# Performance work log

Hardware: AMD Instinct MI355X
Metric: run time of the kernel (lower is better)

The kernel has to match this reference:

```python
import jax, jax.numpy as jnp
import numpy as np
import math

H = 8
D_MODEL = 512
D_K = D_MODEL // H          # 64, per-head value dim
D_QK = D_K // 2             # 32, per-head query/key dim
B, S = 2, 4096


def setup_inputs() -> dict:
    key = jax.random.key(0)
    ks = jax.random.split(key, 20)
    std = 0.02
    inp = {
        'query': jax.random.normal(ks[0], (B, S, D_MODEL), jnp.float32),
        'key':   jax.random.normal(ks[1], (B, S, D_MODEL), jnp.float32),
        'value': jax.random.normal(ks[2], (B, S, D_MODEL), jnp.float32),
        # MLP_q: d_model -> 2*d_model -> d_model/2
        'Wq1': jax.random.normal(ks[3], (D_MODEL, 2 * D_MODEL), jnp.float32) * std,
        'bq1': jnp.zeros((2 * D_MODEL,), jnp.float32),
        'Wq2': jax.random.normal(ks[4], (2 * D_MODEL, D_MODEL // 2), jnp.float32) * std,
        'bq2': jnp.zeros((D_MODEL // 2,), jnp.float32),
        # MLP_k: d_model -> 2*d_model -> d_model/2
        'Wk1': jax.random.normal(ks[5], (D_MODEL, 2 * D_MODEL), jnp.float32) * std,
        'bk1': jnp.zeros((2 * D_MODEL,), jnp.float32),
        'Wk2': jax.random.normal(ks[6], (2 * D_MODEL, D_MODEL // 2), jnp.float32) * std,
        'bk2': jnp.zeros((D_MODEL // 2,), jnp.float32),
        # linear_v and output linear: d_model -> d_model
        'Wv': jax.random.normal(ks[7], (D_MODEL, D_MODEL), jnp.float32) * std,
        'bv': jnp.zeros((D_MODEL,), jnp.float32),
        'Wo': jax.random.normal(ks[8], (D_MODEL, D_MODEL), jnp.float32) * std,
        'bo': jnp.zeros((D_MODEL,), jnp.float32),
    }
    return inp


def reference(query, key, value, Wq1, bq1, Wq2, bq2, Wk1, bk1, Wk2, bk2, Wv, bv, Wo, bo):
    nb = query.shape[0]
    # MLP_q / MLP_k: Linear -> exact GELU -> Linear (torch GELU default is erf)
    q = jax.nn.gelu(query @ Wq1 + bq1, approximate=False) @ Wq2 + bq2   # [B,S,D_MODEL/2]
    k = jax.nn.gelu(key   @ Wk1 + bk1, approximate=False) @ Wk2 + bk2   # [B,S,D_MODEL/2]
    v = value @ Wv + bv                                                  # [B,S,D_MODEL]

    q = q.reshape(nb, -1, H, D_QK)   # [B,S,H,d_qk]
    k = k.reshape(nb, -1, H, D_QK)
    v = v.reshape(nb, -1, H, D_K)    # [B,S,H,d_k]

    # scores scaled by sqrt(d_qk) since query.size(-1) == d_k//2 in the original
    scores = jnp.einsum('bqhd,bkhd->bhqk', q, k) / math.sqrt(D_QK)  # [B,H,S,S]
    p = jax.nn.softmax(scores, axis=-1)
    x = jnp.einsum('bhqk,bkhd->bqhd', p, v).reshape(nb, -1, H * D_K)  # [B,S,D_MODEL]
    return x @ Wo + bo
```

## Files before the change

kernel.cpp:

```cpp
#include <hip/hip_runtime.h>
#include <math.h>

typedef __attribute__((ext_vector_type(8))) short short8;
typedef __bf16 bf16x8 __attribute__((ext_vector_type(8)));
typedef __attribute__((ext_vector_type(4))) float f32x4;
typedef __attribute__((ext_vector_type(16))) float f32x16;
typedef __attribute__((ext_vector_type(4))) unsigned uint4v;

__device__ inline short f2bf(float f) {
    unsigned u = __builtin_bit_cast(unsigned, f);
    u += 0x7fff + ((u >> 16) & 1);
    return (short)(u >> 16);
}
__device__ inline float bf2f(short h) {
    return __builtin_bit_cast(float, ((unsigned)(unsigned short)h) << 16);
}
__device__ inline float gelu_f(float x) {
    return 0.5f * x * (1.f + erff(x * 0.70710678118654752f));
}

__global__ __launch_bounds__(256) void prep_all(
    const float* __restrict__ q, const float* __restrict__ k,
    const float* __restrict__ v,
    short* __restrict__ qc, short* __restrict__ kc, short* __restrict__ vc,
    const float* __restrict__ Wq1, const float* __restrict__ Wk1,
    const float* __restrict__ Wq2, const float* __restrict__ Wk2,
    const float* __restrict__ Wv,  const float* __restrict__ Wo,
    short* __restrict__ Wq1t, short* __restrict__ Wk1t,
    short* __restrict__ Wq2t, short* __restrict__ Wk2t,
    short* __restrict__ Wvt,  short* __restrict__ Wot)
{
    int id = blockIdx.x;
    if (id < 6144) {
        const float* src = id < 2048 ? q : (id < 4096 ? k : v);
        short* dst = id < 2048 ? qc : (id < 4096 ? kc : vc);
        int blk = id & 2047;
        size_t i = ((size_t)blk * 256 + threadIdx.x) * 8;
        float4 a = *(const float4*)(src + i);
        float4 b = *(const float4*)(src + i + 4);
        short8 o;
        o[0] = f2bf(a.x); o[1] = f2bf(a.y); o[2] = f2bf(a.z); o[3] = f2bf(a.w);
        o[4] = f2bf(b.x); o[5] = f2bf(b.y); o[6] = f2bf(b.z); o[7] = f2bf(b.w);
        *(short8*)(void*)(dst + i) = o;
        return;
    }
    id -= 6144;
    const float* W; short* Wt; int K, N;
    if (id < 512)       { W = Wq1; Wt = Wq1t; K = 512;  N = 1024; }
    else if (id < 1024) { W = Wk1; Wt = Wk1t; K = 512;  N = 1024; id -= 512; }
    else if (id < 1280) { W = Wq2; Wt = Wq2t; K = 1024; N = 256;  id -= 1024; }
    else if (id < 1536) { W = Wk2; Wt = Wk2t; K = 1024; N = 256;  id -= 1280; }
    else if (id < 1792) { W = Wv;  Wt = Wvt;  K = 512;  N = 512;  id -= 1536; }
    else                { W = Wo;  Wt = Wot;  K = 512;  N = 512;  id -= 1792; }
    int nx = N >> 5;
    int n0 = (id % nx) * 32, k0 = (id / nx) * 32;

    __shared__ float T[32][33];
    int tid = threadIdx.x;
    int r = tid >> 3, c4 = (tid & 7) * 4;
    float4 v4 = *(const float4*)&W[(size_t)(k0 + r) * N + n0 + c4];
    T[r][c4 + 0] = v4.x; T[r][c4 + 1] = v4.y; T[r][c4 + 2] = v4.z; T[r][c4 + 3] = v4.w;
    __syncthreads();
    short4 o;
    o.x = f2bf(T[c4 + 0][r]);
    o.y = f2bf(T[c4 + 1][r]);
    o.z = f2bf(T[c4 + 2][r]);
    o.w = f2bf(T[c4 + 3][r]);
    *(short4*)&Wt[(size_t)(n0 + r) * K + k0 + c4] = o;
}

template <int ACT, int OUTF32, int BM, int BN>
__global__ __launch_bounds__(256) void gemm_bt(
    const short* __restrict__ A0, const short* __restrict__ A1,
    const short* __restrict__ B0, const short* __restrict__ B1,
    const float* __restrict__ b0, const float* __restrict__ b1,
    void* C0_, void* C1_,
    float s0, float s1, int nbn, int N, int K)
{
    constexpr int MT = BM / 32;
    constexpr int NT = BN / 32;
    const int z = blockIdx.z;
    const short* A = z ? A1 : A0;
    const short* B = z ? B1 : B0;
    const float* bias = z ? b1 : b0;
    void* C_ = z ? C1_ : C0_;
    const float scale = z ? s1 : s0;

    const int L = blockIdx.x;
    const int xcd = L & 7;
    const int per = L >> 3;
    const int bn = (per % nbn) * BN;
    const int bm = ((per / nbn) * 8 + xcd) * BM;

    const int tid = threadIdx.x;
    const int w = tid >> 6;
    const int lane = tid & 63;
    const int l15 = lane & 15, quad = lane >> 4;
    const int wm = (w >> 1) * (BM / 2), wn = (w & 1) * (BN / 2);

    __shared__ __align__(16) short As[BM * 64];
    __shared__ __align__(16) short Bs[BN * 64];

    f32x4 acc[MT][NT];
#pragma unroll
    for (int mt = 0; mt < MT; ++mt)
#pragma unroll
        for (int nt = 0; nt < NT; ++nt) acc[mt][nt] = (f32x4){0.f, 0.f, 0.f, 0.f};

    for (int k0 = 0; k0 < K; k0 += 64) {
#pragma unroll
        for (int i = 0; i < BM / 32; ++i) {
            int ga = tid + i * 256;
            int row = ga >> 3, g = ga & 7;
            short8 aval = *(const short8*)(const void*)&A[(size_t)(bm + row) * K + k0 + g * 8];
            *(short8*)(void*)&As[row * 64 + ((g ^ (row & 7)) * 8)] = aval;
        }
#pragma unroll
        for (int i = 0; i < BN / 32; ++i) {
            int gb = tid + i * 256;
            int row = gb >> 3, g = gb & 7;
            short8 bval = *(const short8*)(const void*)&B[(size_t)(bn + row) * K + k0 + g * 8];
            *(short8*)(void*)&Bs[row * 64 + ((g ^ (row & 7)) * 8)] = bval;
        }
        __syncthreads();

#pragma unroll
        for (int ks = 0; ks < 2; ++ks) {
            bf16x8 af[MT], bfr[NT];
#pragma unroll
            for (int t = 0; t < MT; ++t) {
                int row = wm + t * 16 + l15;
                af[t] = __builtin_bit_cast(bf16x8,
                    *(const short8*)(const void*)&As[row * 64 + (((ks * 4 + quad) ^ (row & 7)) * 8)]);
            }
#pragma unroll
            for (int t = 0; t < NT; ++t) {
                int row = wn + t * 16 + l15;
                bfr[t] = __builtin_bit_cast(bf16x8,
                    *(const short8*)(const void*)&Bs[row * 64 + (((ks * 4 + quad) ^ (row & 7)) * 8)]);
            }
#pragma unroll
            for (int mt = 0; mt < MT; ++mt)
#pragma unroll
                for (int nt = 0; nt < NT; ++nt)
                    acc[mt][nt] = __builtin_amdgcn_mfma_f32_16x16x32_bf16(af[mt], bfr[nt], acc[mt][nt], 0, 0, 0);
        }
        __syncthreads();
    }

    float bv[NT];
#pragma unroll
    for (int nt = 0; nt < NT; ++nt) bv[nt] = bias[bn + wn + nt * 16 + l15];
#pragma unroll
    for (int mt = 0; mt < MT; ++mt)
#pragma unroll
        for (int r = 0; r < 4; ++r) {
            int row = bm + wm + mt * 16 + quad * 4 + r;
#pragma unroll
            for (int nt = 0; nt < NT; ++nt) {
                float v = acc[mt][nt][r] + bv[nt];
                if (ACT) v = gelu_f(v);
                v *= scale;
                int col = bn + wn + nt * 16 + l15;
                if (OUTF32) ((float*)C_)[(size_t)row * N + col] = v;
                else        ((short*)C_)[(size_t)row * N + col] = f2bf(v);
            }
        }
}

__global__ __launch_bounds__(256) void repack_kv(
    const short* __restrict__ kb, short* __restrict__ kfr,
    const short* __restrict__ vbb, short* __restrict__ vfr)
{
    const int kt = blockIdx.x;
    const int y = blockIdx.y;
    const int t = threadIdx.x;
    __shared__ short Vt[64][72];

    if (y < 16) {
        const int bh = y;
        const int b = bh >> 3, h = bh & 7;
        const int c = t >> 6, l = t & 63;
        const int nt = c >> 1, ks = c & 1;
        int key = kt * 64 + nt * 32 + (l & 31);
        int k = ks * 16 + (l >> 5) * 8;
        short8 v = *(const short8*)(const void*)&kb[(size_t)(b * 4096 + key) * 256 + h * 32 + k];
        *(short8*)(void*)&kfr[((((size_t)bh * 64 + kt) * 4 + c) * 64 + l) * 8] = v;
        return;
    }
    const int bh = y - 16;
    const int b = bh >> 3, h = bh & 7;
#pragma unroll
    for (int it = 0; it < 2; ++it) {
        int idx = t + it * 256;
        int keyr = idx >> 3, c8 = (idx & 7) * 8;
        *(short8*)(void*)&Vt[keyr][c8] =
            *(const short8*)(const void*)&vbb[(size_t)(b * 4096 + kt * 64 + keyr) * 512 + h * 64 + c8];
    }
    __syncthreads();
#pragma unroll
    for (int it = 0; it < 2; ++it) {
        int chunk = (t >> 6) * 2 + it;
        int l = t & 63;
        int dt = chunk >> 2, ks = chunk & 3;
        short8 o;
#pragma unroll
        for (int j = 0; j < 8; ++j)
            o[j] = Vt[ks * 16 + (l >> 5) * 8 + j][dt * 32 + (l & 31)];
        *(short8*)(void*)&vfr[((((size_t)bh * 64 + kt) * 8 + chunk) * 64 + l) * 8] = o;
    }
}

__global__ __launch_bounds__(256) void flash_ks(
    const short* __restrict__ qb, const short* __restrict__ kfr,
    const short* __restrict__ vfr, short* __restrict__ xbb)
{
    const int L = blockIdx.x;
    const int xcd = L & 7;
    const int idx = L >> 3;
    const int bh = xcd * 2 + (idx & 1);
    const int qt = idx >> 1;
    const int b = bh >> 3, h = bh & 7;
    const int w = threadIdx.x >> 6;
    const int qg = w >> 1;
    const int kh = w & 1;
    const int lane = threadIdx.x & 63;
    const int l31 = lane & 31;
    const int half = lane >> 5;

    __shared__ __align__(16) char smem[17408];

    const short* qrow = qb + (size_t)(b * 4096 + qt * 64 + qg * 32 + l31) * 256 + h * 32 + half * 8;
    bf16x8 qf0 = __builtin_bit_cast(bf16x8, *(const short8*)(const void*)qrow);
    bf16x8 qf1 = __builtin_bit_cast(bf16x8, *(const short8*)(const void*)(qrow + 16));

    short8 ones_s;
#pragma unroll
    for (int j = 0; j < 8; ++j) ones_s[j] = (short)0x3F80;
    const bf16x8 onesf = __builtin_bit_cast(bf16x8, ones_s);

    f32x16 O0{}, O1{}, lacc{};

    const short* kbase = kfr + ((size_t)bh * 64) * 4 * 512 + lane * 8;
    const short* vbase = vfr + ((size_t)bh * 64) * 8 * 512 + lane * 8;

#pragma unroll 1
    for (int t = 0; t < 32; ++t) {
        const int kt = kh * 32 + t;
        bf16x8 kc[4], vc[8];
        const short* kp = kbase + (size_t)kt * 4 * 512;
        const short* vp = vbase + (size_t)kt * 8 * 512;
#pragma unroll
        for (int c = 0; c < 4; ++c)
            kc[c] = __builtin_bit_cast(bf16x8, *(const short8*)(const void*)(kp + c * 512));
#pragma unroll
        for (int c = 0; c < 8; ++c)
            vc[c] = __builtin_bit_cast(bf16x8, *(const short8*)(const void*)(vp + c * 512));

        f32x16 zero{};
        f32x16 s0 = __builtin_amdgcn_mfma_f32_32x32x16_bf16(kc[0], qf0, zero, 0, 0, 0);
        s0 = __builtin_amdgcn_mfma_f32_32x32x16_bf16(kc[1], qf1, s0, 0, 0, 0);
        f32x16 s1 = __builtin_amdgcn_mfma_f32_32x32x16_bf16(kc[2], qf0, zero, 0, 0, 0);
        s1 = __builtin_amdgcn_mfma_f32_32x32x16_bf16(kc[3], qf1, s1, 0, 0, 0);

        bf16x8 pf[4];
#pragma unroll
        for (int nt = 0; nt < 2; ++nt) {
            const f32x16& s = nt ? s1 : s0;
            float p0  = __builtin_amdgcn_exp2f(s[0]);
            float p1  = __builtin_amdgcn_exp2f(s[1]);
            float p2  = __builtin_amdgcn_exp2f(s[2]);
            float p3  = __builtin_amdgcn_exp2f(s[3]);
            float p4  = __builtin_amdgcn_exp2f(s[4]);
            float p5  = __builtin_amdgcn_exp2f(s[5]);
            float p6  = __builtin_amdgcn_exp2f(s[6]);
            float p7  = __builtin_amdgcn_exp2f(s[7]);
            float p8  = __builtin_amdgcn_exp2f(s[8]);
            float p9  = __builtin_amdgcn_exp2f(s[9]);
            float p10 = __builtin_amdgcn_exp2f(s[10]);
            float p11 = __builtin_amdgcn_exp2f(s[11]);
            float p12 = __builtin_amdgcn_exp2f(s[12]);
            float p13 = __builtin_amdgcn_exp2f(s[13]);
            float p14 = __builtin_amdgcn_exp2f(s[14]);
            float p15 = __builtin_amdgcn_exp2f(s[15]);
            unsigned D0 = __builtin_amdgcn_perm(
                __builtin_bit_cast(unsigned, p1),  __builtin_bit_cast(unsigned, p0),  0x07060302u);
            unsigned D1 = __builtin_amdgcn_perm(
                __builtin_bit_cast(unsigned, p3),  __builtin_bit_cast(unsigned, p2),  0x07060302u);
            unsigned D2 = __builtin_amdgcn_perm(
                __builtin_bit_cast(unsigned, p5),  __builtin_bit_cast(unsigned, p4),  0x07060302u);
            unsigned D3 = __builtin_amdgcn_perm(
                __builtin_bit_cast(unsigned, p7),  __builtin_bit_cast(unsigned, p6),  0x07060302u);
            unsigned D4 = __builtin_amdgcn_perm(
                __builtin_bit_cast(unsigned, p9),  __builtin_bit_cast(unsigned, p8),  0x07060302u);
            unsigned D5 = __builtin_amdgcn_perm(
                __builtin_bit_cast(unsigned, p11), __builtin_bit_cast(unsigned, p10), 0x07060302u);
            unsigned D6 = __builtin_amdgcn_perm(
                __builtin_bit_cast(unsigned, p13), __builtin_bit_cast(unsigned, p12), 0x07060302u);
            unsigned D7 = __builtin_amdgcn_perm(
                __builtin_bit_cast(unsigned, p15), __builtin_bit_cast(unsigned, p14), 0x07060302u);
            asm("v_permlane32_swap_b32 %0, %1" : "+v"(D0), "+v"(D2));
            asm("v_permlane32_swap_b32 %0, %1" : "+v"(D1), "+v"(D3));
            asm("v_permlane32_swap_b32 %0, %1" : "+v"(D4), "+v"(D6));
            asm("v_permlane32_swap_b32 %0, %1" : "+v"(D5), "+v"(D7));
            uint4v u0; u0[0] = D0; u0[1] = D1; u0[2] = D2; u0[3] = D3;
            uint4v u1; u1[0] = D4; u1[1] = D5; u1[2] = D6; u1[3] = D7;
            pf[2 * nt + 0] = __builtin_bit_cast(bf16x8, u0);
            pf[2 * nt + 1] = __builtin_bit_cast(bf16x8, u1);
        }

#pragma unroll
        for (int ks = 0; ks < 4; ++ks) {
            O0 = __builtin_amdgcn_mfma_f32_32x32x16_bf16(pf[ks], vc[ks], O0, 0, 0, 0);
            O1 = __builtin_amdgcn_mfma_f32_32x32x16_bf16(pf[ks], vc[4 + ks], O1, 0, 0, 0);
            lacc = __builtin_amdgcn_mfma_f32_32x32x16_bf16(pf[ks], onesf, lacc, 0, 0, 0);
        }
    }

    float* redO = (float*)smem;
    float* redl = (float*)(smem + 16896);
    if (l31 == 0) {
#pragma unroll
        for (int r = 0; r < 16; ++r) {
            int q = (r & 3) + 8 * (r >> 2) + 4 * half;
            redl[(qg * 2 + kh) * 32 + q] = lacc[r];
        }
    }
    if (kh == 1) {
        float* Bo = redO + qg * 32 * 66;
#pragma unroll
        for (int r = 0; r < 16; ++r) {
            int q = (r & 3) + 8 * (r >> 2) + 4 * half;
            Bo[q * 66 + l31] = O0[r];
            Bo[q * 66 + 32 + l31] = O1[r];
        }
    }
    __syncthreads();
    if (kh == 0) {
        const float* Bo = redO + qg * 32 * 66;
#pragma unroll
        for (int r = 0; r < 16; ++r) {
            int q = (r & 3) + 8 * (r >> 2) + 4 * half;
            float o0 = O0[r] + Bo[q * 66 + l31];
            float o1 = O1[r] + Bo[q * 66 + 32 + l31];
            float inv = 1.f / (redl[(qg * 2 + 0) * 32 + q] + redl[(qg * 2 + 1) * 32 + q]);
            size_t row = (size_t)(b * 4096 + qt * 64 + qg * 32 + q);
            short* d = xbb + row * 512 + h * 64 + l31;
            d[0] = f2bf(o0 * inv);
            d[32] = f2bf(o1 * inv);
        }
    }
}

extern "C" void kernel_launch(void* const* d_in, const int* in_sizes, int n_in,
                              void* d_out, int out_size, void* d_ws, size_t ws_size,
                              hipStream_t stream)
{
    const float* query = (const float*)d_in[0];
    const float* key   = (const float*)d_in[1];
    const float* value = (const float*)d_in[2];
    const float* Wq1   = (const float*)d_in[3];
    const float* bq1   = (const float*)d_in[4];
    const float* Wq2   = (const float*)d_in[5];
    const float* bq2   = (const float*)d_in[6];
    const float* Wk1   = (const float*)d_in[7];
    const float* bk1   = (const float*)d_in[8];
    const float* Wk2   = (const float*)d_in[9];
    const float* bk2   = (const float*)d_in[10];
    const float* Wv    = (const float*)d_in[11];
    const float* bv    = (const float*)d_in[12];
    const float* Wo    = (const float*)d_in[13];
    const float* bo    = (const float*)d_in[14];
    float* out = (float*)d_out;

    char* ws = (char*)d_ws;
    short* H1q   = (short*)(ws + 0);
    short* H1k   = (short*)(ws + 16777216);
    short* xbb   = (short*)(ws + 0);
    short* qcast = (short*)(ws + 33554432);
    short* kcast = (short*)(ws + 41943040);
    short* vcast = (short*)(ws + 50331648);
    short* qbb   = (short*)(ws + 33554432);
    short* kbb   = (short*)(ws + 37748736);
    short* vbb   = (short*)(ws + 41943040);
    short* kfr   = (short*)(ws + 50331648);
    short* vfr   = (short*)(ws + 54525952);
    short* Wq1t  = (short*)(ws + 62914560);
    short* Wk1t  = (short*)(ws + 63963136);
    short* Wq2t  = (short*)(ws + 65011712);
    short* Wk2t  = (short*)(ws + 65536000);
    short* Wvt   = (short*)(ws + 66060288);
    short* Wot   = (short*)(ws + 66584576);

    dim3 blk(256);
    const float qscale = 0.17677669529663687f * 1.4426950408889634f;

    prep_all<<<dim3(8192), blk, 0, stream>>>(
        query, key, value, qcast, kcast, vcast,
        Wq1, Wk1, Wq2, Wk2, Wv, Wo, Wq1t, Wk1t, Wq2t, Wk2t, Wvt, Wot);

    gemm_bt<1, 0, 128, 128><<<dim3(8 * 64, 1, 2), blk, 0, stream>>>(
        qcast, kcast, Wq1t, Wk1t, bq1, bk1, H1q, H1k, 1.f, 1.f, 8, 1024, 512);
    gemm_bt<0, 0, 64, 64><<<dim3(4 * 128, 1, 2), blk, 0, stream>>>(
        H1q, H1k, Wq2t, Wk2t, bq2, bk2, qbb, kbb, qscale, 1.f, 4, 256, 1024);
    gemm_bt<0, 0, 64, 64><<<dim3(8 * 128, 1, 1), blk, 0, stream>>>(
        vcast, vcast, Wvt, Wvt, bv, bv, vbb, vbb, 1.f, 1.f, 8, 512, 512);
    repack_kv<<<dim3(64, 32), blk, 0, stream>>>(kbb, kfr, vbb, vfr);
    flash_ks<<<dim3(1024), blk, 0, stream>>>(qbb, kfr, vfr, xbb);
    gemm_bt<0, 1, 64, 64><<<dim3(8 * 128, 1, 1), blk, 0, stream>>>(
        xbb, xbb, Wot, Wot, bo, bo, out, out, 1.f, 1.f, 8, 512, 512);
}
```

Measured before the change: 264.4 us.

## Replace ones-MFMA row sum with packed VALU accumulation and hardware bf16 convert

The softmax denominator was computed with an extra MFMA against a ones matrix each key step. It is now a packed f32x2 running sum of the exponentials plus one cross-half permlane swap at the end, which removes a third of the MFMAs in the inner loop and frees the lacc accumulator registers. The truncating byte-perm bf16 packing becomes v_cvt_pk_bf16_f32, and launch bounds now request 4 blocks per SIMD-level occupancy. The denominator is now summed from fp32 probabilities rather than bf16-rounded ones, a slight numeric change, and the extra VALU adds may compete with exp work.

```diff
diff --git a/kernel.cpp b/kernel.cpp
--- a/kernel.cpp
+++ b/kernel.cpp
@@ -4,6 +4,7 @@
 typedef __attribute__((ext_vector_type(8))) short short8;
 typedef __bf16 bf16x8 __attribute__((ext_vector_type(8)));
 typedef __attribute__((ext_vector_type(4))) float f32x4;
+typedef __attribute__((ext_vector_type(2))) float f32x2;
 typedef __attribute__((ext_vector_type(16))) float f32x16;
 typedef __attribute__((ext_vector_type(4))) unsigned uint4v;
 
@@ -211,7 +212,7 @@
     }
 }
 
-__global__ __launch_bounds__(256) void flash_ks(
+__global__ __launch_bounds__(256, 4) void flash_ks(
     const short* __restrict__ qb, const short* __restrict__ kfr,
     const short* __restrict__ vfr, short* __restrict__ xbb)
 {
@@ -234,12 +235,8 @@
     bf16x8 qf0 = __builtin_bit_cast(bf16x8, *(const short8*)(const void*)qrow);
     bf16x8 qf1 = __builtin_bit_cast(bf16x8, *(const short8*)(const void*)(qrow + 16));
 
-    short8 ones_s;
-#pragma unroll
-    for (int j = 0; j < 8; ++j) ones_s[j] = (short)0x3F80;
-    const bf16x8 onesf = __builtin_bit_cast(bf16x8, ones_s);
-
-    f32x16 O0{}, O1{}, lacc{};
+    f32x16 O0{}, O1{};
+    f32x2 lp = (f32x2){0.f, 0.f};
 
     const short* kbase = kfr + ((size_t)bh * 64) * 4 * 512 + lane * 8;
     const short* vbase = vfr + ((size_t)bh * 64) * 8 * 512 + lane * 8;
@@ -283,22 +280,25 @@
             float p13 = __builtin_amdgcn_exp2f(s[13]);
             float p14 = __builtin_amdgcn_exp2f(s[14]);
             float p15 = __builtin_amdgcn_exp2f(s[15]);
-            unsigned D0 = __builtin_amdgcn_perm(
-                __builtin_bit_cast(unsigned, p1),  __builtin_bit_cast(unsigned, p0),  0x07060302u);
-            unsigned D1 = __builtin_amdgcn_perm(
-                __builtin_bit_cast(unsigned, p3),  __builtin_bit_cast(unsigned, p2),  0x07060302u);
-            unsigned D2 = __builtin_amdgcn_perm(
-                __builtin_bit_cast(unsigned, p5),  __builtin_bit_cast(unsigned, p4),  0x07060302u);
-            unsigned D3 = __builtin_amdgcn_perm(
-                __builtin_bit_cast(unsigned, p7),  __builtin_bit_cast(unsigned, p6),  0x07060302u);
-            unsigned D4 = __builtin_amdgcn_perm(
-                __builtin_bit_cast(unsigned, p9),  __builtin_bit_cast(unsigned, p8),  0x07060302u);
-            unsigned D5 = __builtin_amdgcn_perm(
-                __builtin_bit_cast(unsigned, p11), __builtin_bit_cast(unsigned, p10), 0x07060302u);
-            unsigned D6 = __builtin_amdgcn_perm(
-                __builtin_bit_cast(unsigned, p13), __builtin_bit_cast(unsigned, p12), 0x07060302u);
-            unsigned D7 = __builtin_amdgcn_perm(
-                __builtin_bit_cast(unsigned, p15), __builtin_bit_cast(unsigned, p14), 0x07060302u);
+
+            lp += (f32x2){p0,  p1};
+            lp += (f32x2){p2,  p3};
+            lp += (f32x2){p4,  p5};
+            lp += (f32x2){p6,  p7};
+            lp += (f32x2){p8,  p9};
+            lp += (f32x2){p10, p11};
+            lp += (f32x2){p12, p13};
+            lp += (f32x2){p14, p15};
+
+            unsigned D0, D1, D2, D3, D4, D5, D6, D7;
+            asm("v_cvt_pk_bf16_f32 %0, %1, %2" : "=v"(D0) : "v"(p0),  "v"(p1));
+            asm("v_cvt_pk_bf16_f32 %0, %1, %2" : "=v"(D1) : "v"(p2),  "v"(p3));
+            asm("v_cvt_pk_bf16_f32 %0, %1, %2" : "=v"(D2) : "v"(p4),  "v"(p5));
+            asm("v_cvt_pk_bf16_f32 %0, %1, %2" : "=v"(D3) : "v"(p6),  "v"(p7));
+            asm("v_cvt_pk_bf16_f32 %0, %1, %2" : "=v"(D4) : "v"(p8),  "v"(p9));
+            asm("v_cvt_pk_bf16_f32 %0, %1, %2" : "=v"(D5) : "v"(p10), "v"(p11));
+            asm("v_cvt_pk_bf16_f32 %0, %1, %2" : "=v"(D6) : "v"(p12), "v"(p13));
+            asm("v_cvt_pk_bf16_f32 %0, %1, %2" : "=v"(D7) : "v"(p14), "v"(p15));
             asm("v_permlane32_swap_b32 %0, %1" : "+v"(D0), "+v"(D2));
             asm("v_permlane32_swap_b32 %0, %1" : "+v"(D1), "+v"(D3));
             asm("v_permlane32_swap_b32 %0, %1" : "+v"(D4), "+v"(D6));
@@ -313,19 +313,18 @@
         for (int ks = 0; ks < 4; ++ks) {
             O0 = __builtin_amdgcn_mfma_f32_32x32x16_bf16(pf[ks], vc[ks], O0, 0, 0, 0);
             O1 = __builtin_amdgcn_mfma_f32_32x32x16_bf16(pf[ks], vc[4 + ks], O1, 0, 0, 0);
-            lacc = __builtin_amdgcn_mfma_f32_32x32x16_bf16(pf[ks], onesf, lacc, 0, 0, 0);
-        }
-    }
+        }
+    }
+
+    float lsum = lp[0] + lp[1];
+    float lother = lsum;
+    asm("v_permlane32_swap_b32 %0, %1" : "+v"(lsum), "+v"(lother));
+    lsum += lother;
 
     float* redO = (float*)smem;
     float* redl = (float*)(smem + 16896);
-    if (l31 == 0) {
-#pragma unroll
-        for (int r = 0; r < 16; ++r) {
-            int q = (r & 3) + 8 * (r >> 2) + 4 * half;
-            redl[(qg * 2 + kh) * 32 + q] = lacc[r];
-        }
-    }
+    if (half == 0)
+        redl[(qg * 2 + kh) * 32 + l31] = lsum;
     if (kh == 1) {
         float* Bo = redO + qg * 32 * 66;
 #pragma unroll
```

New measurement: 259.5 us. No clear change (-1.9%).
